# Kernel tuning notes

Measured on AMD Instinct MI355X. Metric: run time of the kernel, lower is better.

Reference implementation:

```python
import jax, jax.numpy as jnp
import numpy as np

B, T, F_FEAT = 2048, 128, 8
UO, UI = 128, 64
BN_EPS = 1e-3  # keras BatchNormalization default epsilon


def _lstm(x, Wk, Wr, b):
    """Keras-style LSTM, activation=selu, recurrent_activation=sigmoid.
    x: [B,T,Fin]; Wk: [Fin,4U] (gate order i,f,c,o); Wr: [U,4U]; b: [4U].
    Returns full hidden sequence [B,T,U]. Inference mode (no dropout)."""
    U = Wr.shape[0]
    xz = jnp.einsum('btf,fg->btg', x, Wk) + b        # precompute input projections
    xz = jnp.swapaxes(xz, 0, 1)                      # [T,B,4U]

    def step(carry, zx):
        h, c = carry
        z = zx + h @ Wr                              # [B,4U]
        i, f, g, o = jnp.split(z, 4, axis=-1)
        i = jax.nn.sigmoid(i)
        f = jax.nn.sigmoid(f)
        g = jax.nn.selu(g)
        o = jax.nn.sigmoid(o)
        c = f * c + i * g
        h = o * jax.nn.selu(c)
        return (h, c), h

    h0 = jnp.zeros((x.shape[0], U), x.dtype)
    (_, _), hs = jax.lax.scan(step, (h0, jnp.zeros_like(h0)), xz)
    return jnp.swapaxes(hs, 0, 1)                    # [B,T,U]


def _bn(x, gamma, beta, mean, var):
    # inference-mode BatchNormalization over last (channel) axis
    return (x - mean) * (gamma / jnp.sqrt(var + BN_EPS)) + beta


def setup_inputs() -> dict:
    key = jax.random.key(0)
    ks = jax.random.split(key, 40)
    w = lambda k, shape, s=0.08: jax.random.normal(k, shape, jnp.float32) * s
    inp = {}
    inp['x'] = jax.random.normal(ks[0], (B, T, F_FEAT), jnp.float32)
    # encoder outer LSTM + BN
    inp['Wk1'] = w(ks[1], (F_FEAT, 4 * UO)); inp['Wr1'] = w(ks[2], (UO, 4 * UO)); inp['b1'] = jnp.zeros((4 * UO,), jnp.float32)
    inp['g1'] = 1.0 + w(ks[3], (UO,)); inp['be1'] = w(ks[4], (UO,)); inp['m1'] = w(ks[5], (UO,)); inp['v1'] = 0.5 + jax.random.uniform(ks[6], (UO,), jnp.float32)
    # encoder inner LSTM + BN
    inp['Wk2'] = w(ks[7], (UO, 4 * UI)); inp['Wr2'] = w(ks[8], (UI, 4 * UI)); inp['b2'] = jnp.zeros((4 * UI,), jnp.float32)
    inp['g2'] = 1.0 + w(ks[9], (UI,)); inp['be2'] = w(ks[10], (UI,)); inp['m2'] = w(ks[11], (UI,)); inp['v2'] = 0.5 + jax.random.uniform(ks[12], (UI,), jnp.float32)
    # decoder inner LSTM + BN
    inp['Wk3'] = w(ks[13], (UI, 4 * UI)); inp['Wr3'] = w(ks[14], (UI, 4 * UI)); inp['b3'] = jnp.zeros((4 * UI,), jnp.float32)
    inp['g3'] = 1.0 + w(ks[15], (UI,)); inp['be3'] = w(ks[16], (UI,)); inp['m3'] = w(ks[17], (UI,)); inp['v3'] = 0.5 + jax.random.uniform(ks[18], (UI,), jnp.float32)
    # decoder outer LSTM + BN
    inp['Wk4'] = w(ks[19], (UI, 4 * UO)); inp['Wr4'] = w(ks[20], (UO, 4 * UO)); inp['b4'] = jnp.zeros((4 * UO,), jnp.float32)
    inp['g4'] = 1.0 + w(ks[21], (UO,)); inp['be4'] = w(ks[22], (UO,)); inp['m4'] = w(ks[23], (UO,)); inp['v4'] = 0.5 + jax.random.uniform(ks[24], (UO,), jnp.float32)
    # per-feature TimeDistributed Dense(1) heads fused into one [UO,F] matmul
    inp['Wd'] = w(ks[25], (UO, F_FEAT)); inp['bd'] = jnp.zeros((F_FEAT,), jnp.float32)
    return inp


def reference(x, Wk1, Wr1, b1, g1, be1, m1, v1,
              Wk2, Wr2, b2, g2, be2, m2, v2,
              Wk3, Wr3, b3, g3, be3, m3, v3,
              Wk4, Wr4, b4, g4, be4, m4, v4,
              Wd, bd):
    # encoder
    h = _bn(_lstm(x, Wk1, Wr1, b1), g1, be1, m1, v1)          # [B,T,UO]
    enc = _lstm(h, Wk2, Wr2, b2)[:, -1]                        # return_sequences=False
    enc = _bn(enc, g2, be2, m2, v2)                            # [B,UI]
    # decoder: RepeatVector(T)
    d = jnp.broadcast_to(enc[:, None, :], (enc.shape[0], T, enc.shape[1]))
    d = _bn(_lstm(d, Wk3, Wr3, b3), g3, be3, m3, v3)           # [B,T,UI]
    d = _bn(_lstm(d, Wk4, Wr4, b4), g4, be4, m4, v4)           # [B,T,UO]
    out = jnp.einsum('btu,uf->btf', d, Wd) + bd                # per-feature Dense(1) heads
    return out                                                 # [B,T,F] (== stacked decoded features)
```

## Files before the change

kernel.cpp:

```cpp
#include <hip/hip_runtime.h>
#include <math.h>


typedef _Float16 half8 __attribute__((ext_vector_type(8)));
typedef __attribute__((ext_vector_type(4))) float floatx4;

#define TT 128
#define NF 8
#define BT 8
#define NBLK 256
#define NTH 512

#define FS_Z1 0
#define FS_Z2 160
#define FS_X3 256
#define FS_Z3 288
#define FS_Z4 320
#define FS_DN 512
#define N_FRAGS 516

#define MFMAH(a,b,c) __builtin_amdgcn_mfma_f32_16x16x32_f16((a),(b),(c),0,0,0)
#define PINA(v) asm volatile("" : "+a"(v))

__device__ __forceinline__ float sigmoid_(float x){
    return __builtin_amdgcn_rcpf(1.0f + __expf(-x));
}
__device__ __forceinline__ float selu_(float x){
    const float alpha = 1.6732632423543772f, scale = 1.0507009873554805f;
    return x > 0.0f ? scale*x : scale*alpha*(__expf(x)-1.0f);
}

__global__ void pack_kernel(const float* __restrict__ Wk1, const float* __restrict__ Wr1,
                            const float* __restrict__ Wk2, const float* __restrict__ Wr2,
                            const float* __restrict__ Wk3, const float* __restrict__ Wr3,
                            const float* __restrict__ Wk4, const float* __restrict__ Wr4,
                            const float* __restrict__ Wd, unsigned short* __restrict__ ws)
{
    const int g = blockIdx.x;
    const int l = threadIdx.x;
    int blob, fs, KS;
    if      (g < FS_Z2){ blob = 0; fs = FS_Z1; KS = 5; }
    else if (g < FS_X3){ blob = 1; fs = FS_Z2; KS = 6; }
    else if (g < FS_Z3){ blob = 2; fs = FS_X3; KS = 2; }
    else if (g < FS_Z4){ blob = 3; fs = FS_Z3; KS = 2; }
    else if (g < FS_DN){ blob = 4; fs = FS_Z4; KS = 6; }
    else               { blob = 5; fs = FS_DN; KS = 4; }
    const int fl = g - fs;
    const int tile = fl / KS, kk = fl % KS;
    const int c   = l & 15;
    const int col = tile * 16 + c;
    const int k0  = kk * 32 + (l >> 4) * 8;
    const int oc2 = (2*(tile&1) + (c>>3))*64 + 8*(tile>>1) + (c&7);

    half8 v8;
    #pragma unroll
    for (int j = 0; j < 8; ++j){
        const int k = k0 + j;
        float v = 0.0f;
        switch (blob){
            case 0: v = (k < 128) ? Wr1[k*512 + col] : (k < 136 ? Wk1[(k-128)*512 + col] : 0.0f); break;
            case 1: v = (k < 128) ? Wk2[k*256 + oc2] : Wr2[(k-128)*256 + oc2]; break;
            case 2: v = Wk3[k*256 + col]; break;
            case 3: v = Wr3[k*256 + col]; break;
            case 4: v = (k < 64) ? Wk4[k*512 + col] : Wr4[(k-64)*512 + col]; break;
            case 5: v = (col < 8) ? Wd[k*8 + col] : 0.0f; break;
        }
        v8[j] = (_Float16)v;
    }
    *(half8*)(ws + (size_t)g*512 + l*8) = v8;
}

__global__ __launch_bounds__(NTH, 1) void lstm_ae_mfma(
    const float* __restrict__ x,
    const float* __restrict__ b1, const float* __restrict__ b2,
    const float* __restrict__ b3, const float* __restrict__ b4,
    const float* __restrict__ bd,
    const float* __restrict__ g1, const float* __restrict__ be1, const float* __restrict__ m1, const float* __restrict__ v1,
    const float* __restrict__ g2, const float* __restrict__ be2, const float* __restrict__ m2, const float* __restrict__ v2,
    const float* __restrict__ g3, const float* __restrict__ be3, const float* __restrict__ m3, const float* __restrict__ v3,
    const float* __restrict__ g4, const float* __restrict__ be4, const float* __restrict__ m4, const float* __restrict__ v4,
    const unsigned short* __restrict__ WS,
    float* __restrict__ out)
{
    __shared__ __align__(16) _Float16 AZ1[2][5][512];
    __shared__ __align__(16) _Float16 AH1B[2][4][512];
    __shared__ __align__(16) _Float16 AH2[2][2][512];
    __shared__ __align__(16) _Float16 AH3[2][2][512];
    __shared__ __align__(16) _Float16 AH3B[2][2][512];
    __shared__ __align__(16) _Float16 AH4[2][4][512];
    __shared__ __align__(16) _Float16 AH4B[2][4][512];

    const int tid = threadIdx.x;
    const int w = tid >> 6, l = tid & 63;
    const int l15 = l & 15, q = l >> 4;
    const int h8 = (l15 >> 3) & 1;
    const int b0 = blockIdx.x * BT;
    const int arow0 = 4*q;

    const int u1 = 16*w + l15;
    const int kk1 = u1 >> 5;
    const int sbase1 = ((u1>>3)&3)*128 + (u1&7);
    const float s1v = g1[u1]*rsqrtf(v1[u1]+1e-3f), t1v = be1[u1]-m1[u1]*s1v;
    const float s4v = g4[u1]*rsqrtf(v4[u1]+1e-3f), t4v = be4[u1]-m4[u1]*s4v;

    const int u2n = 8*w + (l15 & 7);
    const int s2w = (w&3)*128 + (arow0 + h8)*8 + (l15&7);
    const float s2v = g2[u2n]*rsqrtf(v2[u2n]+1e-3f), t2v = be2[u2n]-m2[u2n]*s2v;

    const int u3 = 16*(w&3) + l15;
    const int kk3 = u3 >> 5;
    const int sbase3 = ((u3>>3)&3)*128 + (u3&7);
    const float s3v = g3[u3]*rsqrtf(v3[u3]+1e-3f);
    const float t3v = be3[u3]-m3[u3]*s3v;

    float z1b[4], z4b[4], z2b[2];
    #pragma unroll
    for (int i = 0; i < 4; ++i){
        z1b[i] = b1[(w + 8*i)*16 + l15];
        z4b[i] = b4[(w + 8*i)*16 + l15];
    }
    #pragma unroll
    for (int i = 0; i < 2; ++i)
        z2b[i] = b2[(2*i + h8)*64 + u2n];
    float b3v[4];
    #pragma unroll
    for (int i = 0; i < 4; ++i)
        b3v[i] = (w < 4) ? b3[((w&3) + 4*i)*16 + l15] : 0.0f;
    const float bdv = (w == 4 && l15 < 8) ? bd[l15] : 0.0f;

    half8 wz1[4][5], wz2[2][6];
    #pragma unroll
    for (int i = 0; i < 4; ++i)
        #pragma unroll
        for (int kk = 0; kk < 5; ++kk){
            wz1[i][kk] = *(const half8*)(WS + (size_t)(FS_Z1 + (w+8*i)*5 + kk)*512 + l*8);
            PINA(wz1[i][kk]);
        }
    #pragma unroll
    for (int i = 0; i < 2; ++i)
        #pragma unroll
        for (int kk = 0; kk < 6; ++kk){
            wz2[i][kk] = *(const half8*)(WS + (size_t)(FS_Z2 + (2*w+i)*6 + kk)*512 + l*8);
            PINA(wz2[i][kk]);
        }

    for (int i = tid; i < 2560; i += NTH) ((int*)AZ1)[i] = 0;
    for (int i = tid; i < 2048; i += NTH){
        ((int*)AH1B)[i] = 0; ((int*)AH4)[i] = 0; ((int*)AH4B)[i] = 0;
    }
    for (int i = tid; i < 1024; i += NTH){
        ((int*)AH2)[i] = 0; ((int*)AH3)[i] = 0; ((int*)AH3B)[i] = 0;
    }
    if (tid < 64){
        const int br = tid >> 3, ar = (br & 1) + 4*(br >> 1);
        AZ1[0][4][ar*8 + (tid&7)] = (_Float16)x[(size_t)(b0+br)*(TT*NF) + (tid&7)];
    }
    float c1r[2] = {0,0}, c4r[2] = {0,0}, c3r[2] = {0,0};
    float c2r = 0.0f, h2last = 0.0f;
    __syncthreads();

    for (int t = -1; t < TT; ++t){
        const int pe = t & 1;
        if (t + 1 < TT){
            float xnext = 0.0f;
            if (tid < 64 && t + 2 < TT)
                xnext = x[(size_t)(b0+(tid>>3))*(TT*NF) + (size_t)(t+2)*NF + (tid&7)];

            floatx4 acc[4];
            #pragma unroll
            for (int i = 0; i < 4; ++i) acc[i] = (floatx4){z1b[i],z1b[i],z1b[i],z1b[i]};
            #pragma unroll
            for (int kk = 0; kk < 5; ++kk){
                half8 a = *(const half8*)&AZ1[pe^1][kk][l*8];
                #pragma unroll
                for (int i = 0; i < 4; ++i)
                    acc[i] = MFMAH(a, wz1[i][kk], acc[i]);
            }
            #pragma unroll
            for (int r = 0; r < 2; ++r){
                float ig = sigmoid_(acc[0][r]);
                float fg = sigmoid_(acc[1][r]);
                float gg = selu_(acc[2][r]);
                float og = sigmoid_(acc[3][r]);
                float c = fg*c1r[r] + ig*gg; c1r[r] = c;
                float h = og*selu_(c);
                const int s = sbase1 + (arow0 + r)*8;
                AZ1[pe][kk1][s]    = (_Float16)h;
                AH1B[pe^1][kk1][s] = (_Float16)(h*s1v + t1v);
            }
            if (tid < 64 && t + 2 < TT){
                const int br = tid >> 3, ar = (br & 1) + 4*(br >> 1);
                AZ1[pe][4][ar*8 + (tid&7)] = (_Float16)xnext;
            }
        }
        if (t >= 0){
            floatx4 a2[2];
            #pragma unroll
            for (int i = 0; i < 2; ++i) a2[i] = (floatx4){z2b[i],z2b[i],z2b[i],z2b[i]};
            #pragma unroll
            for (int kk = 0; kk < 6; ++kk){
                half8 a = (kk < 4) ? *(const half8*)&AH1B[pe][kk][l*8]
                                   : *(const half8*)&AH2[pe][kk-4][l*8];
                #pragma unroll
                for (int i = 0; i < 2; ++i)
                    a2[i] = MFMAH(a, wz2[i][kk], a2[i]);
            }
            float keep0 = h8 ? a2[0][1] : a2[0][0];
            float keep1 = h8 ? a2[1][1] : a2[1][0];
            float give0 = h8 ? a2[0][0] : a2[0][1];
            float give1 = h8 ? a2[1][0] : a2[1][1];
            float e0 = __shfl_xor(give0, 8);
            float e1 = __shfl_xor(give1, 8);
            float zi = h8 ? e0    : keep0;
            float zf = h8 ? keep0 : e0;
            float zg = h8 ? e1    : keep1;
            float zo = h8 ? keep1 : e1;
            float ig = sigmoid_(zi);
            float fg = sigmoid_(zf);
            float gg = selu_(zg);
            float og = sigmoid_(zo);
            float c = fg*c2r + ig*gg; c2r = c;
            h2last = og*selu_(c);
            AH2[pe^1][w>>2][s2w] = (_Float16)h2last;
        }
        __syncthreads();
    }

    AH3B[1][w>>2][s2w] = (_Float16)(h2last*s2v + t2v);
    __syncthreads();
    floatx4 xz3r[4];
    if (w < 4){
        #pragma unroll
        for (int i = 0; i < 4; ++i) xz3r[i] = (floatx4){b3v[i],b3v[i],b3v[i],b3v[i]};
        #pragma unroll
        for (int kk = 0; kk < 2; ++kk){
            half8 a = *(const half8*)&AH3B[1][kk][l*8];
            #pragma unroll
            for (int i = 0; i < 4; ++i){
                half8 b = *(const half8*)(WS + (size_t)(FS_X3 + ((w&3)+4*i)*2 + kk)*512 + l*8);
                xz3r[i] = MFMAH(a, b, xz3r[i]);
            }
        }
    }

    half8 wz4[4][6], wrole[8];
    #pragma unroll
    for (int i = 0; i < 4; ++i)
        #pragma unroll
        for (int kk = 0; kk < 6; ++kk){
            wz4[i][kk] = *(const half8*)(WS + (size_t)(FS_Z4 + (w+8*i)*6 + kk)*512 + l*8);
            PINA(wz4[i][kk]);
        }
    if (w < 4){
        #pragma unroll
        for (int i = 0; i < 4; ++i)
            #pragma unroll
            for (int kk = 0; kk < 2; ++kk){
                wrole[i*2+kk] = *(const half8*)(WS + (size_t)(FS_Z3 + ((w&3)+4*i)*2 + kk)*512 + l*8);
                PINA(wrole[i*2+kk]);
            }
    } else if (w == 4){
        #pragma unroll
        for (int kk = 0; kk < 4; ++kk){
            wrole[kk] = *(const half8*)(WS + (size_t)(FS_DN + kk)*512 + l*8);
            PINA(wrole[kk]);
        }
    }
    __syncthreads();

    for (int t = -1; t < TT; ++t){
        const int pd = t & 1;
        if (w < 4 && t + 1 < TT){
            floatx4 a3[4];
            #pragma unroll
            for (int i = 0; i < 4; ++i) a3[i] = xz3r[i];
            #pragma unroll
            for (int kk = 0; kk < 2; ++kk){
                half8 a = *(const half8*)&AH3[pd^1][kk][l*8];
                #pragma unroll
                for (int i = 0; i < 4; ++i)
                    a3[i] = MFMAH(a, wrole[i*2+kk], a3[i]);
            }
            #pragma unroll
            for (int r = 0; r < 2; ++r){
                float ig = sigmoid_(a3[0][r]);
                float fg = sigmoid_(a3[1][r]);
                float gg = selu_(a3[2][r]);
                float og = sigmoid_(a3[3][r]);
                float c = fg*c3r[r] + ig*gg; c3r[r] = c;
                float h = og*selu_(c);
                const int s = sbase3 + (arow0 + r)*8;
                AH3[pd][kk3][s]     = (_Float16)h;
                AH3B[pd^1][kk3][s]  = (_Float16)(h*s3v + t3v);
            }
        } else if (w == 4 && t > 0){
            floatx4 ad = (floatx4){bdv,bdv,bdv,bdv};
            #pragma unroll
            for (int kk = 0; kk < 4; ++kk){
                half8 a = *(const half8*)&AH4B[pd^1][kk][l*8];
                ad = MFMAH(a, wrole[kk], ad);
            }
            if (l15 < 8){
                #pragma unroll
                for (int r = 0; r < 2; ++r)
                    out[(size_t)(b0 + 2*q + r)*(TT*NF) + (size_t)(t-1)*NF + l15] = ad[r];
            }
        }
        if (t >= 0){
            floatx4 a4[4];
            #pragma unroll
            for (int i = 0; i < 4; ++i) a4[i] = (floatx4){z4b[i],z4b[i],z4b[i],z4b[i]};
            #pragma unroll
            for (int kk = 0; kk < 6; ++kk){
                half8 a = (kk < 2) ? *(const half8*)&AH3B[pd][kk][l*8]
                                   : *(const half8*)&AH4[pd][kk-2][l*8];
                #pragma unroll
                for (int i = 0; i < 4; ++i)
                    a4[i] = MFMAH(a, wz4[i][kk], a4[i]);
            }
            #pragma unroll
            for (int r = 0; r < 2; ++r){
                float ig = sigmoid_(a4[0][r]);
                float fg = sigmoid_(a4[1][r]);
                float gg = selu_(a4[2][r]);
                float og = sigmoid_(a4[3][r]);
                float c = fg*c4r[r] + ig*gg; c4r[r] = c;
                float h = og*selu_(c);
                const int s = sbase1 + (arow0 + r)*8;
                AH4[pd^1][kk1][s] = (_Float16)h;
                AH4B[pd][kk1][s]  = (_Float16)(h*s4v + t4v);
            }
        }
        __syncthreads();
    }

    if (w == 4){
        floatx4 ad = (floatx4){bdv,bdv,bdv,bdv};
        #pragma unroll
        for (int kk = 0; kk < 4; ++kk){
            half8 a = *(const half8*)&AH4B[(TT-1)&1][kk][l*8];
            ad = MFMAH(a, wrole[kk], ad);
        }
        if (l15 < 8){
            #pragma unroll
            for (int r = 0; r < 2; ++r)
                out[(size_t)(b0 + 2*q + r)*(TT*NF) + (size_t)(TT-1)*NF + l15] = ad[r];
        }
    }
}

extern "C" void kernel_launch(void* const* d_in, const int* in_sizes, int n_in,
                              void* d_out, int out_size, void* d_ws, size_t ws_size,
                              hipStream_t stream) {
    const float* x   = (const float*)d_in[0];
    const float* Wk1 = (const float*)d_in[1];  const float* Wr1 = (const float*)d_in[2];
    const float* b1  = (const float*)d_in[3];
    const float* g1  = (const float*)d_in[4];  const float* be1 = (const float*)d_in[5];
    const float* m1  = (const float*)d_in[6];  const float* v1  = (const float*)d_in[7];
    const float* Wk2 = (const float*)d_in[8];  const float* Wr2 = (const float*)d_in[9];
    const float* b2  = (const float*)d_in[10];
    const float* g2  = (const float*)d_in[11]; const float* be2 = (const float*)d_in[12];
    const float* m2  = (const float*)d_in[13]; const float* v2  = (const float*)d_in[14];
    const float* Wk3 = (const float*)d_in[15]; const float* Wr3 = (const float*)d_in[16];
    const float* b3  = (const float*)d_in[17];
    const float* g3  = (const float*)d_in[18]; const float* be3 = (const float*)d_in[19];
    const float* m3  = (const float*)d_in[20]; const float* v3  = (const float*)d_in[21];
    const float* Wk4 = (const float*)d_in[22]; const float* Wr4 = (const float*)d_in[23];
    const float* b4  = (const float*)d_in[24];
    const float* g4  = (const float*)d_in[25]; const float* be4 = (const float*)d_in[26];
    const float* m4  = (const float*)d_in[27]; const float* v4  = (const float*)d_in[28];
    const float* Wd  = (const float*)d_in[29]; const float* bd  = (const float*)d_in[30];

    unsigned short* ws = (unsigned short*)d_ws;

    pack_kernel<<<dim3(N_FRAGS), dim3(64), 0, stream>>>(Wk1, Wr1, Wk2, Wr2, Wk3, Wr3,
                                                        Wk4, Wr4, Wd, ws);
    lstm_ae_mfma<<<dim3(NBLK), dim3(NTH), 0, stream>>>(
        x, b1, b2, b3, b4, bd,
        g1, be1, m1, v1, g2, be2, m2, v2,
        g3, be3, m3, v3, g4, be4, m4, v4,
        (const unsigned short*)ws, (float*)d_out);
}
```

Before: 438.1 us.

## Fold decoder BatchNorms into next-layer weights and split LSTM3 across all waves

The decoder BN3 and BN4 scale factors are folded into the packed Wk4 and Wd fp16 weights, and their shifts into the biases by a new foldbias kernel. This removes the per-step BN writes and the AH3B/AH4B shared buffers. Layer-3 LSTM work, previously done only by 4 of the 8 waves, is now spread over all 8 waves using the same gate-exchange shuffle scheme as layer 2. The layer-3 hidden fragments are loaded once per step and reused by the layer-4 MFMAs. It adds a tiny extra launch, and scaling the weights before fp16 conversion changes rounding slightly.

```diff
diff --git a/kernel.cpp b/kernel.cpp
--- a/kernel.cpp
+++ b/kernel.cpp
@@ -17,6 +17,7 @@
 #define FS_Z3 288
 #define FS_Z4 320
 #define FS_DN 512
+#define FS_EXT 516
 #define N_FRAGS 516
 
 #define MFMAH(a,b,c) __builtin_amdgcn_mfma_f32_16x16x32_f16((a),(b),(c),0,0,0)
@@ -34,7 +35,10 @@
                             const float* __restrict__ Wk2, const float* __restrict__ Wr2,
                             const float* __restrict__ Wk3, const float* __restrict__ Wr3,
                             const float* __restrict__ Wk4, const float* __restrict__ Wr4,
-                            const float* __restrict__ Wd, unsigned short* __restrict__ ws)
+                            const float* __restrict__ Wd,
+                            const float* __restrict__ g3, const float* __restrict__ v3,
+                            const float* __restrict__ g4, const float* __restrict__ v4,
+                            unsigned short* __restrict__ ws)
 {
     const int g = blockIdx.x;
     const int l = threadIdx.x;
@@ -60,14 +64,43 @@
         switch (blob){
             case 0: v = (k < 128) ? Wr1[k*512 + col] : (k < 136 ? Wk1[(k-128)*512 + col] : 0.0f); break;
             case 1: v = (k < 128) ? Wk2[k*256 + oc2] : Wr2[(k-128)*256 + oc2]; break;
-            case 2: v = Wk3[k*256 + col]; break;
-            case 3: v = Wr3[k*256 + col]; break;
-            case 4: v = (k < 64) ? Wk4[k*512 + col] : Wr4[(k-64)*512 + col]; break;
-            case 5: v = (col < 8) ? Wd[k*8 + col] : 0.0f; break;
+            case 2: v = Wk3[k*256 + oc2]; break;
+            case 3: v = Wr3[k*256 + oc2]; break;
+            case 4: v = (k < 64) ? Wk4[k*512 + col] * (g3[k]*rsqrtf(v3[k]+1e-3f))
+                                 : Wr4[(k-64)*512 + col]; break;
+            case 5: v = (col < 8) ? Wd[k*8 + col] * (g4[k]*rsqrtf(v4[k]+1e-3f)) : 0.0f; break;
         }
         v8[j] = (_Float16)v;
     }
     *(half8*)(ws + (size_t)g*512 + l*8) = v8;
+}
+
+__global__ void foldbias_kernel(const float* __restrict__ b4, const float* __restrict__ bd,
+                                const float* __restrict__ g3, const float* __restrict__ be3,
+                                const float* __restrict__ m3, const float* __restrict__ v3,
+                                const float* __restrict__ g4, const float* __restrict__ be4,
+                                const float* __restrict__ m4, const float* __restrict__ v4,
+                                const float* __restrict__ Wk4, const float* __restrict__ Wd,
+                                unsigned short* __restrict__ ws)
+{
+    float* wsf = (float*)(ws + (size_t)FS_EXT*512);
+    const int tid = threadIdx.x;
+    float s = b4[tid];
+    for (int k = 0; k < 64; ++k){
+        float s3 = g3[k]*rsqrtf(v3[k]+1e-3f);
+        float t3 = be3[k] - m3[k]*s3;
+        s += t3 * Wk4[k*512 + tid];
+    }
+    wsf[tid] = s;
+    if (tid < 8){
+        float d = bd[tid];
+        for (int k = 0; k < 128; ++k){
+            float s4 = g4[k]*rsqrtf(v4[k]+1e-3f);
+            float t4 = be4[k] - m4[k]*s4;
+            d += t4 * Wd[k*8 + tid];
+        }
+        wsf[512 + tid] = d;
+    }
 }
 
 __global__ __launch_bounds__(NTH, 1) void lstm_ae_mfma(
@@ -86,9 +119,8 @@
     __shared__ __align__(16) _Float16 AH1B[2][4][512];
     __shared__ __align__(16) _Float16 AH2[2][2][512];
     __shared__ __align__(16) _Float16 AH3[2][2][512];
-    __shared__ __align__(16) _Float16 AH3B[2][2][512];
     __shared__ __align__(16) _Float16 AH4[2][4][512];
-    __shared__ __align__(16) _Float16 AH4B[2][4][512];
+    __shared__ __align__(16) _Float16 ENC[2][512];
 
     const int tid = threadIdx.x;
     const int w = tid >> 6, l = tid & 63;
@@ -101,32 +133,25 @@
     const int kk1 = u1 >> 5;
     const int sbase1 = ((u1>>3)&3)*128 + (u1&7);
     const float s1v = g1[u1]*rsqrtf(v1[u1]+1e-3f), t1v = be1[u1]-m1[u1]*s1v;
-    const float s4v = g4[u1]*rsqrtf(v4[u1]+1e-3f), t4v = be4[u1]-m4[u1]*s4v;
-
-    const int u2n = 8*w + (l15 & 7);
+
+    const int un = 8*w + (l15 & 7);
     const int s2w = (w&3)*128 + (arow0 + h8)*8 + (l15&7);
-    const float s2v = g2[u2n]*rsqrtf(v2[u2n]+1e-3f), t2v = be2[u2n]-m2[u2n]*s2v;
-
-    const int u3 = 16*(w&3) + l15;
-    const int kk3 = u3 >> 5;
-    const int sbase3 = ((u3>>3)&3)*128 + (u3&7);
-    const float s3v = g3[u3]*rsqrtf(v3[u3]+1e-3f);
-    const float t3v = be3[u3]-m3[u3]*s3v;
-
-    float z1b[4], z4b[4], z2b[2];
+    const float s2v = g2[un]*rsqrtf(v2[un]+1e-3f), t2v = be2[un]-m2[un]*s2v;
+
+    const float* wsf = (const float*)(WS + (size_t)FS_EXT*512);
+
+    float z1b[4], z4b[4], z2b[2], z3b[2];
     #pragma unroll
     for (int i = 0; i < 4; ++i){
         z1b[i] = b1[(w + 8*i)*16 + l15];
-        z4b[i] = b4[(w + 8*i)*16 + l15];
-    }
-    #pragma unroll
-    for (int i = 0; i < 2; ++i)
-        z2b[i] = b2[(2*i + h8)*64 + u2n];
-    float b3v[4];
-    #pragma unroll
-    for (int i = 0; i < 4; ++i)
-        b3v[i] = (w < 4) ? b3[((w&3) + 4*i)*16 + l15] : 0.0f;
-    const float bdv = (w == 4 && l15 < 8) ? bd[l15] : 0.0f;
+        z4b[i] = wsf[(w + 8*i)*16 + l15];
+    }
+    #pragma unroll
+    for (int i = 0; i < 2; ++i){
+        z2b[i] = b2[(2*i + h8)*64 + un];
+        z3b[i] = b3[(2*i + h8)*64 + un];
+    }
+    const float bdv = (w == 4 && l15 < 8) ? wsf[512 + l15] : 0.0f;
 
     half8 wz1[4][5], wz2[2][6];
     #pragma unroll
@@ -145,18 +170,15 @@
         }
 
     for (int i = tid; i < 2560; i += NTH) ((int*)AZ1)[i] = 0;
-    for (int i = tid; i < 2048; i += NTH){
-        ((int*)AH1B)[i] = 0; ((int*)AH4)[i] = 0; ((int*)AH4B)[i] = 0;
-    }
-    for (int i = tid; i < 1024; i += NTH){
-        ((int*)AH2)[i] = 0; ((int*)AH3)[i] = 0; ((int*)AH3B)[i] = 0;
-    }
+    for (int i = tid; i < 2048; i += NTH){ ((int*)AH1B)[i] = 0; ((int*)AH4)[i] = 0; }
+    for (int i = tid; i < 1024; i += NTH){ ((int*)AH2)[i] = 0; ((int*)AH3)[i] = 0; }
+    for (int i = tid; i < 512;  i += NTH) ((int*)ENC)[i] = 0;
     if (tid < 64){
         const int br = tid >> 3, ar = (br & 1) + 4*(br >> 1);
         AZ1[0][4][ar*8 + (tid&7)] = (_Float16)x[(size_t)(b0+br)*(TT*NF) + (tid&7)];
     }
-    float c1r[2] = {0,0}, c4r[2] = {0,0}, c3r[2] = {0,0};
-    float c2r = 0.0f, h2last = 0.0f;
+    float c1r[2] = {0,0}, c4r[2] = {0,0};
+    float c2r = 0.0f, c3r = 0.0f, h2last = 0.0f;
     __syncthreads();
 
     for (int t = -1; t < TT; ++t){
@@ -226,24 +248,22 @@
         __syncthreads();
     }
 
-    AH3B[1][w>>2][s2w] = (_Float16)(h2last*s2v + t2v);
+    ENC[w>>2][s2w] = (_Float16)(h2last*s2v + t2v);
     __syncthreads();
-    floatx4 xz3r[4];
-    if (w < 4){
-        #pragma unroll
-        for (int i = 0; i < 4; ++i) xz3r[i] = (floatx4){b3v[i],b3v[i],b3v[i],b3v[i]};
-        #pragma unroll
-        for (int kk = 0; kk < 2; ++kk){
-            half8 a = *(const half8*)&AH3B[1][kk][l*8];
-            #pragma unroll
-            for (int i = 0; i < 4; ++i){
-                half8 b = *(const half8*)(WS + (size_t)(FS_X3 + ((w&3)+4*i)*2 + kk)*512 + l*8);
-                xz3r[i] = MFMAH(a, b, xz3r[i]);
-            }
-        }
-    }
-
-    half8 wz4[4][6], wrole[8];
+    floatx4 xz3r[2];
+    #pragma unroll
+    for (int i = 0; i < 2; ++i) xz3r[i] = (floatx4){z3b[i],z3b[i],z3b[i],z3b[i]};
+    #pragma unroll
+    for (int kk = 0; kk < 2; ++kk){
+        half8 a = *(const half8*)&ENC[kk][l*8];
+        #pragma unroll
+        for (int i = 0; i < 2; ++i){
+            half8 b = *(const half8*)(WS + (size_t)(FS_X3 + (2*w+i)*2 + kk)*512 + l*8);
+            xz3r[i] = MFMAH(a, b, xz3r[i]);
+        }
+    }
+
+    half8 wz4[4][6], wr3[2][2], wd4[4];
     #pragma unroll
     for (int i = 0; i < 4; ++i)
         #pragma unroll
@@ -251,54 +271,58 @@
             wz4[i][kk] = *(const half8*)(WS + (size_t)(FS_Z4 + (w+8*i)*6 + kk)*512 + l*8);
             PINA(wz4[i][kk]);
         }
-    if (w < 4){
-        #pragma unroll
-        for (int i = 0; i < 4; ++i)
-            #pragma unroll
-            for (int kk = 0; kk < 2; ++kk){
-                wrole[i*2+kk] = *(const half8*)(WS + (size_t)(FS_Z3 + ((w&3)+4*i)*2 + kk)*512 + l*8);
-                PINA(wrole[i*2+kk]);
-            }
-    } else if (w == 4){
+    #pragma unroll
+    for (int i = 0; i < 2; ++i)
+        #pragma unroll
+        for (int kk = 0; kk < 2; ++kk){
+            wr3[i][kk] = *(const half8*)(WS + (size_t)(FS_Z3 + (2*w+i)*2 + kk)*512 + l*8);
+            PINA(wr3[i][kk]);
+        }
+    if (w == 4){
         #pragma unroll
         for (int kk = 0; kk < 4; ++kk){
-            wrole[kk] = *(const half8*)(WS + (size_t)(FS_DN + kk)*512 + l*8);
-            PINA(wrole[kk]);
+            wd4[kk] = *(const half8*)(WS + (size_t)(FS_DN + kk)*512 + l*8);
+            PINA(wd4[kk]);
         }
     }
     __syncthreads();
 
     for (int t = -1; t < TT; ++t){
         const int pd = t & 1;
-        if (w < 4 && t + 1 < TT){
-            floatx4 a3[4];
-            #pragma unroll
-            for (int i = 0; i < 4; ++i) a3[i] = xz3r[i];
-            #pragma unroll
-            for (int kk = 0; kk < 2; ++kk){
-                half8 a = *(const half8*)&AH3[pd^1][kk][l*8];
-                #pragma unroll
-                for (int i = 0; i < 4; ++i)
-                    a3[i] = MFMAH(a, wrole[i*2+kk], a3[i]);
-            }
-            #pragma unroll
-            for (int r = 0; r < 2; ++r){
-                float ig = sigmoid_(a3[0][r]);
-                float fg = sigmoid_(a3[1][r]);
-                float gg = selu_(a3[2][r]);
-                float og = sigmoid_(a3[3][r]);
-                float c = fg*c3r[r] + ig*gg; c3r[r] = c;
-                float h = og*selu_(c);
-                const int s = sbase3 + (arow0 + r)*8;
-                AH3[pd][kk3][s]     = (_Float16)h;
-                AH3B[pd^1][kk3][s]  = (_Float16)(h*s3v + t3v);
-            }
-        } else if (w == 4 && t > 0){
+        half8 a3k0 = *(const half8*)&AH3[pd^1][0][l*8];
+        half8 a3k1 = *(const half8*)&AH3[pd^1][1][l*8];
+        if (t + 1 < TT){
+            floatx4 a3[2];
+            a3[0] = xz3r[0]; a3[1] = xz3r[1];
+            #pragma unroll
+            for (int i = 0; i < 2; ++i){
+                a3[i] = MFMAH(a3k0, wr3[i][0], a3[i]);
+                a3[i] = MFMAH(a3k1, wr3[i][1], a3[i]);
+            }
+            float keep0 = h8 ? a3[0][1] : a3[0][0];
+            float keep1 = h8 ? a3[1][1] : a3[1][0];
+            float give0 = h8 ? a3[0][0] : a3[0][1];
+            float give1 = h8 ? a3[1][0] : a3[1][1];
+            float e0 = __shfl_xor(give0, 8);
+            float e1 = __shfl_xor(give1, 8);
+            float zi = h8 ? e0    : keep0;
+            float zf = h8 ? keep0 : e0;
+            float zg = h8 ? e1    : keep1;
+            float zo = h8 ? keep1 : e1;
+            float ig = sigmoid_(zi);
+            float fg = sigmoid_(zf);
+            float gg = selu_(zg);
+            float og = sigmoid_(zo);
+            float c = fg*c3r + ig*gg; c3r = c;
+            float h = og*selu_(c);
+            AH3[pd][w>>2][s2w] = (_Float16)h;
+        }
+        if (w == 4 && t > 0){
             floatx4 ad = (floatx4){bdv,bdv,bdv,bdv};
             #pragma unroll
             for (int kk = 0; kk < 4; ++kk){
-                half8 a = *(const half8*)&AH4B[pd^1][kk][l*8];
-                ad = MFMAH(a, wrole[kk], ad);
+                half8 a = *(const half8*)&AH4[pd][kk][l*8];
+                ad = MFMAH(a, wd4[kk], ad);
             }
             if (l15 < 8){
                 #pragma unroll
@@ -311,9 +335,13 @@
             #pragma unroll
             for (int i = 0; i < 4; ++i) a4[i] = (floatx4){z4b[i],z4b[i],z4b[i],z4b[i]};
             #pragma unroll
-            for (int kk = 0; kk < 6; ++kk){
-                half8 a = (kk < 2) ? *(const half8*)&AH3B[pd][kk][l*8]
-                                   : *(const half8*)&AH4[pd][kk-2][l*8];
+            for (int i = 0; i < 4; ++i){
+                a4[i] = MFMAH(a3k0, wz4[i][0], a4[i]);
+                a4[i] = MFMAH(a3k1, wz4[i][1], a4[i]);
+            }
+            #pragma unroll
+            for (int kk = 2; kk < 6; ++kk){
+                half8 a = *(const half8*)&AH4[pd][kk-2][l*8];
                 #pragma unroll
                 for (int i = 0; i < 4; ++i)
                     a4[i] = MFMAH(a, wz4[i][kk], a4[i]);
@@ -328,7 +356,6 @@
                 float h = og*selu_(c);
                 const int s = sbase1 + (arow0 + r)*8;
                 AH4[pd^1][kk1][s] = (_Float16)h;
-                AH4B[pd][kk1][s]  = (_Float16)(h*s4v + t4v);
             }
         }
         __syncthreads();
@@ -338,8 +365,8 @@
         floatx4 ad = (floatx4){bdv,bdv,bdv,bdv};
         #pragma unroll
         for (int kk = 0; kk < 4; ++kk){
-            half8 a = *(const half8*)&AH4B[(TT-1)&1][kk][l*8];
-            ad = MFMAH(a, wrole[kk], ad);
+            half8 a = *(const half8*)&AH4[0][kk][l*8];
+            ad = MFMAH(a, wd4[kk], ad);
         }
         if (l15 < 8){
             #pragma unroll
@@ -374,7 +401,9 @@
     unsigned short* ws = (unsigned short*)d_ws;
 
     pack_kernel<<<dim3(N_FRAGS), dim3(64), 0, stream>>>(Wk1, Wr1, Wk2, Wr2, Wk3, Wr3,
-                                                        Wk4, Wr4, Wd, ws);
+                                                        Wk4, Wr4, Wd, g3, v3, g4, v4, ws);
+    foldbias_kernel<<<dim3(1), dim3(512), 0, stream>>>(b4, bd, g3, be3, m3, v3,
+                                                       g4, be4, m4, v4, Wk4, Wd, ws);
     lstm_ae_mfma<<<dim3(NBLK), dim3(NTH), 0, stream>>>(
         x, b1, b2, b3, b4, bd,
         g1, be1, m1, v1, g2, be2, m2, v2,
```

Result: no change. 445.0 us (+1.6%).
